# Kernel tuning notes

Measured on AMD Instinct MI355X. Metric: run time of the kernel, lower is better.

The kernel has to match this reference:

```python
import jax, jax.numpy as jnp
import numpy as np

B, N, D = 512, 128, 768
TAU = 1.0            # NeuralSort temperature (allRank default)
COS_W = 0.1          # cosine_loss_weight
EPS = 1e-10          # allRank DEFAULT_EPS
PAD = -1.0           # allRank PADDED_Y_VALUE
SINKHORN_ITERS = 50
SINKHORN_TOL = 1e-6


def setup_inputs() -> dict:
    key = jax.random.key(0)
    kq, kr, ky = jax.random.split(key, 3)
    return {
        "query_embeddings": jax.random.normal(kq, (B, N, D), jnp.float32),
        "response_embeddings": jax.random.normal(kr, (B, N, D), jnp.float32),
        "labels": jax.random.uniform(ky, (B, N), dtype=jnp.float32),
    }


def _cosine_similarity(a, b):
    # torch.cosine_similarity semantics: clamp each norm at 1e-8
    num = jnp.sum(a * b, axis=-1)
    den = jnp.maximum(jnp.linalg.norm(a, axis=-1), 1e-8) * jnp.maximum(jnp.linalg.norm(b, axis=-1), 1e-8)
    return num / den


def _deterministic_neural_sort(s, tau, mask):
    # s: [B, N, 1] scores; mask: [B, N] padding mask (True = padded)
    n = s.shape[1]
    s = jnp.where(mask[:, :, None], -1e8, s)
    A = jnp.abs(s - jnp.swapaxes(s, 1, 2))                       # [B,N,N]
    pair_or = mask[:, :, None] | mask[:, None, :]
    A = jnp.where(pair_or, 0.0, A)
    Bmat = jnp.sum(A, axis=2, keepdims=True)                     # == A @ (1 1^T), broadcasts over cols
    valid = n - jnp.sum(mask, axis=1)                            # [B] number of non-padded items
    idx = jnp.arange(n)
    # per-row scaling vector: (n-m) - 1 - 2*j for j < n-m, else 0
    scaling = jnp.where(idx[None, :] < valid[:, None],
                        (valid[:, None] - 1 - 2 * idx[None, :]).astype(s.dtype), 0.0)
    s0 = jnp.where(mask[:, :, None], 0.0, s)
    C = s0 * scaling[:, None, :]                                 # [B,N,N] = s @ scaling^T
    P_max = jnp.swapaxes(C - Bmat, 1, 2)
    P_max = jnp.where(pair_or, -jnp.inf, P_max)
    P_max = jnp.where(mask[:, :, None] & mask[:, None, :], 1.0, P_max)
    return jax.nn.softmax(P_max / tau, axis=-1)


def _sinkhorn(mat, mask):
    pair_or = mask[:, None, :] | mask[:, :, None]
    pair_and = mask[:, None, :] & mask[:, :, None]
    mat = jnp.where(pair_or, 0.0, mat)
    mat = jnp.where(pair_and, 1.0, mat)

    def step(carry, _):
        m, done = carry
        m1 = m / jnp.maximum(jnp.sum(m, axis=1, keepdims=True), EPS)
        m2 = m1 / jnp.maximum(jnp.sum(m1, axis=2, keepdims=True), EPS)
        conv = (jnp.max(jnp.abs(jnp.sum(m2, axis=2) - 1.0)) < SINKHORN_TOL) & \
               (jnp.max(jnp.abs(jnp.sum(m2, axis=1) - 1.0)) < SINKHORN_TOL)
        new_m = jnp.where(done, m, m2)   # freeze once converged (emulates torch early break)
        return (new_m, done | conv), None

    (mat, _), _ = jax.lax.scan(step, (mat, jnp.array(False)), None, length=SINKHORN_ITERS)
    mat = jnp.where(pair_or, 0.0, mat)
    mat = jnp.where(pair_and, 1.0, mat)
    return mat


def _idcg_at_k(y_true, k):
    # allRank dcg(y_true, y_true, ats=[k]) with powered gains (no padding present)
    sorted_true = -jnp.sort(-y_true, axis=1)                     # descending
    gains = jnp.power(2.0, sorted_true) - 1.0
    discounts = 1.0 / jnp.log2(jnp.arange(y_true.shape[1], dtype=jnp.float32) + 2.0)
    return jnp.cumsum(gains * discounts, axis=1)[:, k - 1]       # [B]


def _forward(query_embeddings, response_embeddings, labels):
    scores = _cosine_similarity(query_embeddings, response_embeddings)   # [B,N]
    y_true = labels
    mask = (y_true == PAD)
    k = N                                                                # k=None -> slate length
    P_hat = _deterministic_neural_sort(scores[:, :, None], TAU, mask)    # [B,N,N]
    P_hat = _sinkhorn(P_hat, mask)
    P_hat = jnp.where(mask[:, :, None] | mask[:, None, :], 0.0, P_hat)
    g = jnp.power(2.0, jnp.where(mask, 0.0, y_true)) - 1.0               # powered relevancies
    ground_truth = jnp.einsum('bij,bj->bi', P_hat, g)                    # approx-sorted gains
    discounts = 1.0 / jnp.log2(jnp.arange(N, dtype=jnp.float32) + 2.0)
    discounted = ground_truth * discounts
    idcg = _idcg_at_k(y_true, k)                                         # [B]
    ndcg = jnp.sum(discounted[:, :k], axis=-1) / (idcg + EPS)
    idcg_zero = idcg == 0.0
    ndcg = jnp.where(idcg_zero, 0.0, ndcg)
    mean_ndcg = jnp.sum(ndcg) / jnp.maximum(jnp.sum(~idcg_zero), 1)
    ndcg_loss = 1.0 - mean_ndcg                                          # 1 + neuralNDCG = 1 - mean_ndcg
    cosine_loss = jnp.mean((scores - labels) ** 2)
    return (1.0 - COS_W) * ndcg_loss + COS_W * cosine_loss


def reference(query_embeddings, response_embeddings, labels):
    return _forward(query_embeddings, response_embeddings, labels)
```

## Files before the change

kernel.cpp:

```cpp
#include <hip/hip_runtime.h>
#include <math.h>

#define BB 512
#define NN 128
#define DD 768
#define SSTR 132
#define S4 (SSTR/4)

__global__ __launch_bounds__(256, 2) void k_ndcg(const float* __restrict__ q,
                                                 const float* __restrict__ r,
                                                 const float* __restrict__ labels,
                                                 float* __restrict__ ndcg_out,
                                                 float* __restrict__ valid_out,
                                                 float* __restrict__ mse_out) {
    extern __shared__ float sm[];
    float* M      = sm;
    float* s_s    = sm + NN * SSTR;
    float* s_B    = s_s + NN;
    float* s_cs   = s_B + NN;
    float* s_rc   = s_cs + NN;
    float* s_g    = s_rc + NN;
    float* s_lab  = s_g + NN;
    float* s_red  = s_lab + NN;
    float* s_mse  = s_red + NN;
    float* s_misc = s_mse + NN;

    const int tid = threadIdx.x;
    const int b   = blockIdx.x;
    const int wv  = tid >> 6;
    const int ln  = tid & 63;
    const int i   = tid >> 1;
    const int h   = tid & 1;
    float4* M4 = (float4*)M;
    const float4* rc4 = (const float4*)s_rc;
    const float4* g4  = (const float4*)s_g;
    const float4* s4a = (const float4*)s_s;
    const float4* B4a = (const float4*)s_B;

    if (tid < NN) {
        float lv = labels[b * NN + tid];
        s_lab[tid] = lv;
        s_g[tid]   = exp2f(lv) - 1.0f;
    }

    const float4* q4 = (const float4*)(q + (size_t)b * NN * DD);
    const float4* r4 = (const float4*)(r + (size_t)b * NN * DD);
    for (int m = 0; m < 32; ++m) {
        const int row = wv + 4 * m;
        const float4* qa = q4 + row * (DD / 4);
        const float4* ra = r4 + row * (DD / 4);
        float qr = 0.f, qq = 0.f, rr2 = 0.f;
#pragma unroll
        for (int k = 0; k < 3; ++k) {
            float4 a = qa[ln + 64 * k];
            float4 c = ra[ln + 64 * k];
            qr  += a.x*c.x + a.y*c.y + a.z*c.z + a.w*c.w;
            qq  += a.x*a.x + a.y*a.y + a.z*a.z + a.w*a.w;
            rr2 += c.x*c.x + c.y*c.y + c.z*c.z + c.w*c.w;
        }
#pragma unroll
        for (int off = 32; off >= 1; off >>= 1) {
            qr  += __shfl_xor(qr, off);
            qq  += __shfl_xor(qq, off);
            rr2 += __shfl_xor(rr2, off);
        }
        if (ln == 0) {
            float den = fmaxf(sqrtf(qq), 1e-8f) * fmaxf(sqrtf(rr2), 1e-8f);
            s_s[row] = qr / den;
        }
    }
    __syncthreads();

    if (tid < NN) {
        float si = s_s[tid];
        float acc = 0.f;
        for (int j = 0; j < NN; ++j) acc += fabsf(si - s_s[j]);
        s_B[tid] = acc;
        float li = s_lab[tid];
        int rank = 0;
        for (int j = 0; j < NN; ++j) {
            float lj = s_lab[j];
            rank += (lj > li) || (lj == li && j < tid);
        }
        s_red[tid] = s_g[tid] / log2f((float)(rank + 2));
        float d = si - li;
        s_mse[tid] = d * d;
    }
    __syncthreads();
    if (tid < 32) {
        float v = s_red[tid] + s_red[tid + 32] + s_red[tid + 64] + s_red[tid + 96];
#pragma unroll
        for (int off = 16; off >= 1; off >>= 1) v += __shfl_xor(v, off);
        if (tid == 0) s_misc[1] = v;
    } else if (tid < 64) {
        int t2 = tid - 32;
        float v = s_mse[t2] + s_mse[t2 + 32] + s_mse[t2 + 64] + s_mse[t2 + 96];
#pragma unroll
        for (int off = 16; off >= 1; off >>= 1) v = v + __shfl_xor(v, off);
        if (t2 == 0) mse_out[b] = v;
    }

    {
        const float scal = (float)(127 - 2 * i);
        float4 w[16];
        float rmax = -1e30f;
#pragma unroll
        for (int k = 0; k < 16; ++k) {
            float4 sv = s4a[16 * h + k];
            float4 Bv = B4a[16 * h + k];
            float4 v;
            v.x = sv.x * scal - Bv.x;
            v.y = sv.y * scal - Bv.y;
            v.z = sv.z * scal - Bv.z;
            v.w = sv.w * scal - Bv.w;
            w[k] = v;
            rmax = fmaxf(rmax, fmaxf(fmaxf(v.x, v.y), fmaxf(v.z, v.w)));
        }
        rmax = fmaxf(rmax, __shfl_xor(rmax, 1));
        float rsum = 0.f;
#pragma unroll
        for (int k = 0; k < 16; ++k) {
            float4 v = w[k];
            v.x = expf(v.x - rmax);
            v.y = expf(v.y - rmax);
            v.z = expf(v.z - rmax);
            v.w = expf(v.w - rmax);
            w[k] = v;
            rsum += v.x + v.y + v.z + v.w;
        }
        rsum += __shfl_xor(rsum, 1);
        float inv = 1.0f / rsum;
#pragma unroll
        for (int k = 0; k < 16; ++k) {
            float4 v = w[k];
            v.x *= inv; v.y *= inv; v.z *= inv; v.w *= inv;
            M4[i * S4 + 16 * h + k] = v;
        }
    }
    __syncthreads();

    const int gg2 = ln >> 3;
    const int cc  = (wv << 3) | (ln & 7);
    for (int it = 0; it < 50; ++it) {
        float4 acc; acc.x = acc.y = acc.z = acc.w = 0.f;
#pragma unroll
        for (int k = 0; k < 16; ++k) {
            float4 v = M4[(gg2 * 16 + k) * S4 + cc];
            acc.x += v.x; acc.y += v.y; acc.z += v.z; acc.w += v.w;
        }
#pragma unroll
        for (int off = 32; off >= 8; off >>= 1) {
            acc.x += __shfl_xor(acc.x, off);
            acc.y += __shfl_xor(acc.y, off);
            acc.z += __shfl_xor(acc.z, off);
            acc.w += __shfl_xor(acc.w, off);
        }
        if (gg2 == 0) ((float4*)s_cs)[cc] = acc;
        __syncthreads();
        if (tid < 64) {
            float c0 = s_cs[tid], c1 = s_cs[tid + 64];
            s_rc[tid]      = 1.0f / fmaxf(c0, 1e-10f);
            s_rc[tid + 64] = 1.0f / fmaxf(c1, 1e-10f);
            float dev = fmaxf(fabsf(c0 - 1.0f), fabsf(c1 - 1.0f));
#pragma unroll
            for (int off = 32; off >= 1; off >>= 1) dev = fmaxf(dev, __shfl_xor(dev, off));
            if (tid == 0) s_misc[0] = dev;
        }
        __syncthreads();
        if (it > 0 && s_misc[0] < 1e-6f) break;

        float4 w[16];
        float acc2 = 0.f;
#pragma unroll
        for (int k = 0; k < 16; ++k) {
            float4 v  = M4[i * S4 + 16 * h + k];
            float4 rv = rc4[16 * h + k];
            v.x *= rv.x; v.y *= rv.y; v.z *= rv.z; v.w *= rv.w;
            w[k] = v;
            acc2 += v.x + v.y + v.z + v.w;
        }
        acc2 += __shfl_xor(acc2, 1);
        float rrv = 1.0f / fmaxf(acc2, 1e-10f);
#pragma unroll
        for (int k = 0; k < 16; ++k) {
            float4 v = w[k];
            v.x *= rrv; v.y *= rrv; v.z *= rrv; v.w *= rrv;
            M4[i * S4 + 16 * h + k] = v;
        }
        __syncthreads();
    }

    {
        float acc = 0.f;
#pragma unroll
        for (int k = 0; k < 16; ++k) {
            float4 v  = M4[i * S4 + 16 * h + k];
            float4 gv = g4[16 * h + k];
            acc += v.x * gv.x + v.y * gv.y + v.z * gv.z + v.w * gv.w;
        }
        acc += __shfl_xor(acc, 1);
        if (h == 0) s_red[i] = acc / log2f((float)(i + 2));
    }
    __syncthreads();
    if (tid < 32) {
        float v = s_red[tid] + s_red[tid + 32] + s_red[tid + 64] + s_red[tid + 96];
#pragma unroll
        for (int off = 16; off >= 1; off >>= 1) v += __shfl_xor(v, off);
        if (tid == 0) {
            float idcg = s_misc[1];
            bool zero = (idcg == 0.0f);
            ndcg_out[b]  = zero ? 0.0f : v / (idcg + 1e-10f);
            valid_out[b] = zero ? 0.0f : 1.0f;
        }
    }
}

__global__ __launch_bounds__(256) void k_final(const float* __restrict__ ndcg,
                                               const float* __restrict__ valid,
                                               const float* __restrict__ mse,
                                               float* __restrict__ out) {
    __shared__ float red[3][4];
    const int tid = threadIdx.x;
    const int lane = tid & 63, wv = tid >> 6;
    float nsum = ndcg[tid] + ndcg[tid + 256];
    float vsum = valid[tid] + valid[tid + 256];
    float msum = mse[tid] + mse[tid + 256];
#pragma unroll
    for (int off = 32; off >= 1; off >>= 1) {
        nsum += __shfl_xor(nsum, off);
        vsum += __shfl_xor(vsum, off);
        msum += __shfl_xor(msum, off);
    }
    if (lane == 0) { red[0][wv] = nsum; red[1][wv] = vsum; red[2][wv] = msum; }
    __syncthreads();
    if (tid == 0) {
        float n = red[0][0] + red[0][1] + red[0][2] + red[0][3];
        float v = red[1][0] + red[1][1] + red[1][2] + red[1][3];
        float m = red[2][0] + red[2][1] + red[2][2] + red[2][3];
        float mean_ndcg = n / fmaxf(v, 1.0f);
        out[0] = 0.9f * (1.0f - mean_ndcg) + 0.1f * (m / (float)(BB * NN));
    }
}

extern "C" void kernel_launch(void* const* d_in, const int* in_sizes, int n_in,
                              void* d_out, int out_size, void* d_ws, size_t ws_size,
                              hipStream_t stream) {
    const float* q   = (const float*)d_in[0];
    const float* r   = (const float*)d_in[1];
    const float* lab = (const float*)d_in[2];
    float* ndcg  = (float*)d_ws;
    float* valid = ndcg + BB;
    float* mse   = valid + BB;
    float* out   = (float*)d_out;

    const size_t smem = (size_t)(NN * SSTR + 8 * NN + 16) * sizeof(float);
    hipFuncSetAttribute((const void*)k_ndcg,
                        hipFuncAttributeMaxDynamicSharedMemorySize, (int)smem);
    k_ndcg<<<BB, 256, smem, stream>>>(q, r, lab, ndcg, valid, mse);

    k_final<<<1, 256, 0, stream>>>(ndcg, valid, mse, out);
}
```

Before: 497.8 us.

## Run Sinkhorn as diagonal scaling vectors over register-resident kernel rows/columns

Drops the explicit 128x128 shared-memory matrix. Sinkhorn is rewritten as an equivalent diag(u)·K·diag(v) scaling: each thread keeps its row and column slices of the exponentiated kernel in registers, and every iteration only updates the u and v vectors through dot products. This removes the per-iteration full-matrix read and write traffic in LDS and the large shared allocation, which may allow more resident blocks. In exchange the column exponentials are computed twice, register pressure rises, and rounding differs slightly from explicit normalisation.

```diff
diff --git a/kernel.cpp b/kernel.cpp
--- a/kernel.cpp
+++ b/kernel.cpp
@@ -4,8 +4,6 @@
 #define BB 512
 #define NN 128
 #define DD 768
-#define SSTR 132
-#define S4 (SSTR/4)
 
 __global__ __launch_bounds__(256, 2) void k_ndcg(const float* __restrict__ q,
                                                  const float* __restrict__ r,
@@ -13,29 +11,25 @@
                                                  float* __restrict__ ndcg_out,
                                                  float* __restrict__ valid_out,
                                                  float* __restrict__ mse_out) {
-    extern __shared__ float sm[];
-    float* M      = sm;
-    float* s_s    = sm + NN * SSTR;
-    float* s_B    = s_s + NN;
-    float* s_cs   = s_B + NN;
-    float* s_rc   = s_cs + NN;
-    float* s_g    = s_rc + NN;
-    float* s_lab  = s_g + NN;
-    float* s_red  = s_lab + NN;
-    float* s_mse  = s_red + NN;
-    float* s_misc = s_mse + NN;
+    __shared__ float s_s[NN];
+    __shared__ float s_B[NN];
+    __shared__ float s_lab[NN];
+    __shared__ float s_g[NN];
+    __shared__ float s_u[NN];
+    __shared__ float s_v[NN];
+    __shared__ float s_rmax[NN];
+    __shared__ float s_red[NN];
+    __shared__ float s_mse[NN];
+    __shared__ float s_gv[NN];
+    __shared__ float s_wred[4];
+    __shared__ float s_idcg[1];
 
     const int tid = threadIdx.x;
     const int b   = blockIdx.x;
     const int wv  = tid >> 6;
     const int ln  = tid & 63;
-    const int i   = tid >> 1;
+    const int p   = tid >> 1;
     const int h   = tid & 1;
-    float4* M4 = (float4*)M;
-    const float4* rc4 = (const float4*)s_rc;
-    const float4* g4  = (const float4*)s_g;
-    const float4* s4a = (const float4*)s_s;
-    const float4* B4a = (const float4*)s_B;
 
     if (tid < NN) {
         float lv = labels[b * NN + tid];
@@ -91,7 +85,7 @@
         float v = s_red[tid] + s_red[tid + 32] + s_red[tid + 64] + s_red[tid + 96];
 #pragma unroll
         for (int off = 16; off >= 1; off >>= 1) v += __shfl_xor(v, off);
-        if (tid == 0) s_misc[1] = v;
+        if (tid == 0) s_idcg[0] = v;
     } else if (tid < 64) {
         int t2 = tid - 32;
         float v = s_mse[t2] + s_mse[t2 + 32] + s_mse[t2 + 64] + s_mse[t2 + 96];
@@ -100,9 +94,12 @@
         if (t2 == 0) mse_out[b] = v;
     }
 
+    float u_p;
+    float4 kr[16];
     {
-        const float scal = (float)(127 - 2 * i);
-        float4 w[16];
+        const float scal = (float)(127 - 2 * p);
+        const float4* s4a = (const float4*)s_s;
+        const float4* B4a = (const float4*)s_B;
         float rmax = -1e30f;
 #pragma unroll
         for (int k = 0; k < 16; ++k) {
@@ -113,93 +110,95 @@
             v.y = sv.y * scal - Bv.y;
             v.z = sv.z * scal - Bv.z;
             v.w = sv.w * scal - Bv.w;
-            w[k] = v;
+            kr[k] = v;
             rmax = fmaxf(rmax, fmaxf(fmaxf(v.x, v.y), fmaxf(v.z, v.w)));
         }
         rmax = fmaxf(rmax, __shfl_xor(rmax, 1));
         float rsum = 0.f;
 #pragma unroll
         for (int k = 0; k < 16; ++k) {
-            float4 v = w[k];
+            float4 v = kr[k];
             v.x = expf(v.x - rmax);
             v.y = expf(v.y - rmax);
             v.z = expf(v.z - rmax);
             v.w = expf(v.w - rmax);
-            w[k] = v;
+            kr[k] = v;
             rsum += v.x + v.y + v.z + v.w;
         }
         rsum += __shfl_xor(rsum, 1);
-        float inv = 1.0f / rsum;
-#pragma unroll
-        for (int k = 0; k < 16; ++k) {
-            float4 v = w[k];
-            v.x *= inv; v.y *= inv; v.z *= inv; v.w *= inv;
-            M4[i * S4 + 16 * h + k] = v;
-        }
-    }
-    __syncthreads();
-
-    const int gg2 = ln >> 3;
-    const int cc  = (wv << 3) | (ln & 7);
+        u_p = 1.0f / rsum;
+        if (h == 0) { s_u[p] = u_p; s_rmax[p] = rmax; }
+    }
+    __syncthreads();
+
+    float4 kc[16];
+    {
+        const float sp = s_s[p];
+        const float Bp = s_B[p];
+        const float4* rm4 = (const float4*)s_rmax;
+#pragma unroll
+        for (int k = 0; k < 16; ++k) {
+            float4 rm = rm4[16 * h + k];
+            const float base = (float)(127 - 2 * (64 * h + 4 * k));
+            float4 e;
+            e.x = expf(sp * base          - Bp - rm.x);
+            e.y = expf(sp * (base - 2.f)  - Bp - rm.y);
+            e.z = expf(sp * (base - 4.f)  - Bp - rm.z);
+            e.w = expf(sp * (base - 6.f)  - Bp - rm.w);
+            kc[k] = e;
+        }
+    }
+
+    float v_p = 1.0f;
+    const float4* u4 = (const float4*)s_u;
+    const float4* v4 = (const float4*)s_v;
     for (int it = 0; it < 50; ++it) {
-        float4 acc; acc.x = acc.y = acc.z = acc.w = 0.f;
-#pragma unroll
-        for (int k = 0; k < 16; ++k) {
-            float4 v = M4[(gg2 * 16 + k) * S4 + cc];
-            acc.x += v.x; acc.y += v.y; acc.z += v.z; acc.w += v.w;
-        }
-#pragma unroll
-        for (int off = 32; off >= 8; off >>= 1) {
-            acc.x += __shfl_xor(acc.x, off);
-            acc.y += __shfl_xor(acc.y, off);
-            acc.z += __shfl_xor(acc.z, off);
-            acc.w += __shfl_xor(acc.w, off);
-        }
-        if (gg2 == 0) ((float4*)s_cs)[cc] = acc;
+        float a = 0.f;
+#pragma unroll
+        for (int k = 0; k < 16; ++k) {
+            float4 uu = u4[16 * h + k];
+            float4 kk = kc[k];
+            a += uu.x*kk.x + uu.y*kk.y + uu.z*kk.z + uu.w*kk.w;
+        }
+        a += __shfl_xor(a, 1);
+        float cs  = v_p * a;
+        float dev = fabsf(cs - 1.0f);
+#pragma unroll
+        for (int off = 2; off <= 32; off <<= 1) dev = fmaxf(dev, __shfl_xor(dev, off));
+        if (ln == 0) s_wred[wv] = dev;
         __syncthreads();
-        if (tid < 64) {
-            float c0 = s_cs[tid], c1 = s_cs[tid + 64];
-            s_rc[tid]      = 1.0f / fmaxf(c0, 1e-10f);
-            s_rc[tid + 64] = 1.0f / fmaxf(c1, 1e-10f);
-            float dev = fmaxf(fabsf(c0 - 1.0f), fabsf(c1 - 1.0f));
-#pragma unroll
-            for (int off = 32; off >= 1; off >>= 1) dev = fmaxf(dev, __shfl_xor(dev, off));
-            if (tid == 0) s_misc[0] = dev;
-        }
+        float devmax = fmaxf(fmaxf(s_wred[0], s_wred[1]), fmaxf(s_wred[2], s_wred[3]));
+        if (it > 0 && devmax < 1e-6f) break;
+        v_p = v_p / fmaxf(cs, 1e-10f);
+        if (h == 0) s_v[p] = v_p;
         __syncthreads();
-        if (it > 0 && s_misc[0] < 1e-6f) break;
-
-        float4 w[16];
-        float acc2 = 0.f;
-#pragma unroll
-        for (int k = 0; k < 16; ++k) {
-            float4 v  = M4[i * S4 + 16 * h + k];
-            float4 rv = rc4[16 * h + k];
-            v.x *= rv.x; v.y *= rv.y; v.z *= rv.z; v.w *= rv.w;
-            w[k] = v;
-            acc2 += v.x + v.y + v.z + v.w;
-        }
-        acc2 += __shfl_xor(acc2, 1);
-        float rrv = 1.0f / fmaxf(acc2, 1e-10f);
-#pragma unroll
-        for (int k = 0; k < 16; ++k) {
-            float4 v = w[k];
-            v.x *= rrv; v.y *= rrv; v.z *= rrv; v.w *= rrv;
-            M4[i * S4 + 16 * h + k] = v;
-        }
+        float bb = 0.f;
+#pragma unroll
+        for (int k = 0; k < 16; ++k) {
+            float4 vv = v4[16 * h + k];
+            float4 kk = kr[k];
+            bb += vv.x*kk.x + vv.y*kk.y + vv.z*kk.z + vv.w*kk.w;
+        }
+        bb += __shfl_xor(bb, 1);
+        float rsm = u_p * bb;
+        u_p = u_p / fmaxf(rsm, 1e-10f);
+        if (h == 0) s_u[p] = u_p;
         __syncthreads();
     }
 
+    if (tid < NN) s_gv[tid] = s_g[tid] * s_v[tid];
+    __syncthreads();
     {
+        const float4* gv4 = (const float4*)s_gv;
         float acc = 0.f;
 #pragma unroll
         for (int k = 0; k < 16; ++k) {
-            float4 v  = M4[i * S4 + 16 * h + k];
-            float4 gv = g4[16 * h + k];
-            acc += v.x * gv.x + v.y * gv.y + v.z * gv.z + v.w * gv.w;
+            float4 gv = gv4[16 * h + k];
+            float4 kk = kr[k];
+            acc += kk.x*gv.x + kk.y*gv.y + kk.z*gv.z + kk.w*gv.w;
         }
         acc += __shfl_xor(acc, 1);
-        if (h == 0) s_red[i] = acc / log2f((float)(i + 2));
+        if (h == 0) s_red[p] = u_p * acc / log2f((float)(p + 2));
     }
     __syncthreads();
     if (tid < 32) {
@@ -207,7 +206,7 @@
 #pragma unroll
         for (int off = 16; off >= 1; off >>= 1) v += __shfl_xor(v, off);
         if (tid == 0) {
-            float idcg = s_misc[1];
+            float idcg = s_idcg[0];
             bool zero = (idcg == 0.0f);
             ndcg_out[b]  = zero ? 0.0f : v / (idcg + 1e-10f);
             valid_out[b] = zero ? 0.0f : 1.0f;
@@ -253,10 +252,6 @@
     float* mse   = valid + BB;
     float* out   = (float*)d_out;
 
-    const size_t smem = (size_t)(NN * SSTR + 8 * NN + 16) * sizeof(float);
-    hipFuncSetAttribute((const void*)k_ndcg,
-                        hipFuncAttributeMaxDynamicSharedMemorySize, (int)smem);
-    k_ndcg<<<BB, 256, smem, stream>>>(q, r, lab, ndcg, valid, mse);
-
+    k_ndcg<<<BB, 256, 0, stream>>>(q, r, lab, ndcg, valid, mse);
     k_final<<<1, 256, 0, stream>>>(ndcg, valid, mse, out);
 }
```

Result: faster. 451.3 us (-9.3%).
